# Performance work log

Measured on AMD Instinct MI355X. Metric: run time of the kernel, lower is better.

Reference implementation:

```python
import jax, jax.numpy as jnp
import numpy as np

D_MODEL = 2048
N_HEADS = 16
KV_HEADS = 4
HEAD_DIM = D_MODEL // N_HEADS            # 128
GROUP = N_HEADS // KV_HEADS              # 4
KV_WIDTH = KV_HEADS * HEAD_DIM           # 512
B, T = 2, 2048


def setup_inputs() -> dict:
    key = jax.random.key(0)
    ks = jax.random.split(key, 5)
    s = 0.02
    x = jax.random.normal(ks[0], (B, T, D_MODEL), dtype=jnp.float32)
    attn_mask = jnp.tril(jnp.ones((T, T), dtype=bool))  # causal
    qkv_w = jax.random.normal(ks[1], (D_MODEL, D_MODEL + 2 * KV_WIDTH), dtype=jnp.float32) * s
    qkv_b = jax.random.normal(ks[2], (D_MODEL + 2 * KV_WIDTH,), dtype=jnp.float32) * s
    proj_w = jax.random.normal(ks[3], (D_MODEL, D_MODEL), dtype=jnp.float32) * s
    proj_b = jax.random.normal(ks[4], (D_MODEL,), dtype=jnp.float32) * s
    return {"x": x, "attn_mask": attn_mask, "qkv_w": qkv_w, "qkv_b": qkv_b,
            "proj_w": proj_w, "proj_b": proj_b}


def reference(x, attn_mask, qkv_w, qkv_b, proj_w, proj_b):
    b, t, c = x.shape
    qkv = x @ qkv_w + qkv_b                               # [b,t,3072]
    q = qkv[..., :D_MODEL]
    k = qkv[..., D_MODEL:D_MODEL + KV_WIDTH]
    v = qkv[..., D_MODEL + KV_WIDTH:]
    # q: [b, kv_heads, group, t, d]; k,v: [b, kv_heads, t, d]
    q = q.reshape(b, t, KV_HEADS, GROUP, HEAD_DIM).transpose(0, 2, 3, 1, 4)
    k = k.reshape(b, t, KV_HEADS, HEAD_DIM).transpose(0, 2, 1, 3)
    v = v.reshape(b, t, KV_HEADS, HEAD_DIM).transpose(0, 2, 1, 3)
    scale = 1.0 / jnp.sqrt(jnp.asarray(HEAD_DIM, dtype=x.dtype))
    att = jnp.einsum('bkgtd,bksd->bkgts', q, k) * scale   # [b,kv,g,t,t]
    att = jnp.where(attn_mask, att, jnp.asarray(-jnp.inf, dtype=att.dtype))
    att = jax.nn.softmax(att, axis=-1)
    out = jnp.einsum('bkgts,bksd->bkgtd', att, v)         # [b,kv,g,t,d]
    out = out.transpose(0, 3, 1, 2, 4).reshape(b, t, c)
    return out @ proj_w + proj_b
```

## Files before the change

### kernel.cpp

```cpp
#include <hip/hip_runtime.h>
#include <cstdint>
#include <cstddef>

#define D_MODEL 2048
#define T_SEQ   2048
#define BATCH   2
#define N_HEADS 16
#define KV_HEADS 4
#define HEAD_DIM 128
#define QKV_N   3072
#define ROWS    (BATCH * T_SEQ)

typedef float  floatx4 __attribute__((ext_vector_type(4)));
typedef short  shortx8 __attribute__((ext_vector_type(8)));
typedef __bf16 bf16x8  __attribute__((ext_vector_type(8)));

typedef const void __attribute__((address_space(1))) gvoid_t;
typedef void __attribute__((address_space(3)))       svoid_t;

__device__ __forceinline__ floatx4 mfma16(shortx8 a, shortx8 b, floatx4 c) {
  return __builtin_amdgcn_mfma_f32_16x16x32_bf16(
      __builtin_bit_cast(bf16x8, a), __builtin_bit_cast(bf16x8, b), c, 0, 0, 0);
}

__device__ __forceinline__ unsigned short f2bf(float f) {
  union { float f; unsigned int u; } v; v.f = f;
  unsigned int u = v.u;
  u += 0x7fffu + ((u >> 16) & 1u);
  return (unsigned short)(u >> 16);
}

__device__ __forceinline__ unsigned short f2bf_hw(float f) {
  return __builtin_bit_cast(unsigned short, (__bf16)f);
}

__global__ void cvt_x(const float* __restrict__ in, unsigned short* __restrict__ out, int n4) {
  int i = blockIdx.x * blockDim.x + threadIdx.x;
  if (i >= n4) return;
  float4 v = ((const float4*)in)[i];
  ushort4 o;
  o.x = f2bf(v.x); o.y = f2bf(v.y); o.z = f2bf(v.z); o.w = f2bf(v.w);
  ((ushort4*)out)[i] = o;
}

__global__ void transpose_cvt(const float* __restrict__ W, unsigned short* __restrict__ Wt,
                              int K, int N) {
  __shared__ float tile[32][33];
  int n0 = blockIdx.x * 32, k0 = blockIdx.y * 32;
  int tx = threadIdx.x, ty = threadIdx.y;
  #pragma unroll
  for (int i = 0; i < 32; i += 8)
    tile[ty + i][tx] = W[(size_t)(k0 + ty + i) * N + n0 + tx];
  __syncthreads();
  #pragma unroll
  for (int i = 0; i < 32; i += 8)
    Wt[(size_t)(n0 + ty + i) * K + k0 + tx] = f2bf(tile[tx][ty + i]);
}

__global__ void build_kt(const unsigned short* __restrict__ qkv, unsigned short* __restrict__ kst) {
  int o = blockIdx.x * blockDim.x + threadIdx.x;
  int t   = o & 2047;
  int d8  = (o >> 11) & 15;
  int kvh = (o >> 15) & 3;
  int b   = o >> 17;
  uint4 v = *(const uint4*)(qkv + (size_t)(b * T_SEQ + t) * QKV_N
                            + D_MODEL + kvh * HEAD_DIM + d8 * 8);
  *(uint4*)(kst + (size_t)o * 8) = v;
}

__global__ void build_vt(const unsigned short* __restrict__ qkv, unsigned short* __restrict__ vst) {
  int o = blockIdx.x * blockDim.x + threadIdx.x;
  int d   = o & 127;
  int t8  = (o >> 7) & 255;
  int kvh = (o >> 15) & 3;
  int b   = o >> 17;
  const unsigned short* src = qkv + (size_t)(b * T_SEQ + t8 * 8) * QKV_N
                              + D_MODEL + 512 + kvh * HEAD_DIM + d;
  union { unsigned short s[8]; uint4 v; } tmp;
  #pragma unroll
  for (int j = 0; j < 8; ++j) tmp.s[j] = src[(size_t)j * QKV_N];
  *(uint4*)(vst + (size_t)o * 8) = tmp.v;
}

__global__ __launch_bounds__(512, 2) void gemm256(
    const unsigned short* __restrict__ A,
    const unsigned short* __restrict__ Bt,
    const float* __restrict__ bias,
    void* __restrict__ Cout,
    int M, int N, int K, int c_bf16)
{
  __shared__ __align__(16) unsigned short lds[65536];
  const int tid  = threadIdx.x;
  const int wave = tid >> 6, lane = tid & 63;
  const int quad = lane >> 4, l16 = lane & 15;
  const int wr = wave >> 2, wc = wave & 3;
  const int bm = blockIdx.y * 256, bn = blockIdx.x * 256;
  const int NT = K >> 6;

  const int r0 = tid >> 3;
  const int cx = (tid & 7) ^ (r0 & 7);
  const size_t K64 = (size_t)64 * K;
  const unsigned short* a_src = A  + (size_t)(bm + r0) * K + cx * 8;
  const unsigned short* b_src = Bt + (size_t)(bn + r0) * K + cx * 8;
  const int wOff = wave * 512;

  #define LDSA_(buf, half) (lds + (((buf) << 1) + (half)) * 8192)
  #define LDSB_(buf, half) (lds + 32768 + (((buf) << 1) + (half)) * 8192)
  #define KOFF(h, t) ((size_t)(h) * 128 * K + (size_t)(t) * 64)
  #define STAGE(srcbase, ldshalf, koff) do {                                          \
    __builtin_amdgcn_global_load_lds((gvoid_t*)((srcbase) + (koff)),                  \
        (svoid_t*)((ldshalf) + wOff), 16, 0, 0);                                      \
    __builtin_amdgcn_global_load_lds((gvoid_t*)((srcbase) + (koff) + K64),            \
        (svoid_t*)((ldshalf) + wOff + 4096), 16, 0, 0);                               \
  } while (0)

  const int rowA = (wr * 64 + l16) * 64;
  const int rowB = (wc * 32 + l16) * 64;
  const int xo0 = ((quad)     ^ (l16 & 7)) * 8;
  const int xo1 = ((4 + quad) ^ (l16 & 7)) * 8;

  floatx4 acc[8][4] = {};
  shortx8 Afr[4][2];
  shortx8 Bfr[4][2];

  STAGE(a_src, LDSA_(0, 0), KOFF(0, 0));
  STAGE(b_src, LDSB_(0, 0), KOFF(0, 0));
  STAGE(b_src, LDSB_(0, 1), KOFF(1, 0));
  STAGE(a_src, LDSA_(0, 1), KOFF(1, 0));
  if (NT > 1) {
    STAGE(a_src, LDSA_(1, 0), KOFF(0, 1));
    STAGE(b_src, LDSB_(1, 0), KOFF(0, 1));
    STAGE(b_src, LDSB_(1, 1), KOFF(1, 1));
  }

  for (int t = 0; t < NT; ++t) {
    const int buf = t & 1;
    unsigned short* sA0 = LDSA_(buf, 0);
    unsigned short* sA1 = LDSA_(buf, 1);
    unsigned short* sB0 = LDSB_(buf, 0);
    unsigned short* sB1 = LDSB_(buf, 1);

    if (t == NT - 1) asm volatile("s_waitcnt vmcnt(0)" ::: "memory");
    else             asm volatile("s_waitcnt vmcnt(6)" ::: "memory");
    __builtin_amdgcn_s_barrier();
    #pragma unroll
    for (int mi = 0; mi < 4; ++mi) {
      Afr[mi][0] = *(const shortx8*)(sA0 + rowA + mi * 1024 + xo0);
      Afr[mi][1] = *(const shortx8*)(sA0 + rowA + mi * 1024 + xo1);
    }
    #pragma unroll
    for (int ni = 0; ni < 2; ++ni) {
      Bfr[ni][0] = *(const shortx8*)(sB0 + rowB + ni * 1024 + xo0);
      Bfr[ni][1] = *(const shortx8*)(sB0 + rowB + ni * 1024 + xo1);
    }
    if (t + 1 < NT) STAGE(a_src, LDSA_(buf ^ 1, 1), KOFF(1, t + 1));
    asm volatile("s_waitcnt lgkmcnt(0)" ::: "memory");
    __builtin_amdgcn_s_setprio(1);
    #pragma unroll
    for (int ks = 0; ks < 2; ++ks)
      #pragma unroll
      for (int mi = 0; mi < 4; ++mi)
        #pragma unroll
        for (int ni = 0; ni < 2; ++ni)
          acc[mi][ni] = mfma16(Afr[mi][ks], Bfr[ni][ks], acc[mi][ni]);
    __builtin_amdgcn_s_setprio(0);
    __builtin_amdgcn_s_barrier();

    #pragma unroll
    for (int ni = 0; ni < 2; ++ni) {
      Bfr[2 + ni][0] = *(const shortx8*)(sB1 + rowB + ni * 1024 + xo0);
      Bfr[2 + ni][1] = *(const shortx8*)(sB1 + rowB + ni * 1024 + xo1);
    }
    if (t + 2 < NT) STAGE(a_src, LDSA_(buf, 0), KOFF(0, t + 2));
    __builtin_amdgcn_s_barrier();
    asm volatile("s_waitcnt lgkmcnt(0)" ::: "memory");
    __builtin_amdgcn_s_setprio(1);
    #pragma unroll
    for (int ks = 0; ks < 2; ++ks)
      #pragma unroll
      for (int mi = 0; mi < 4; ++mi)
        #pragma unroll
        for (int ni = 0; ni < 2; ++ni)
          acc[mi][2 + ni] = mfma16(Afr[mi][ks], Bfr[2 + ni][ks], acc[mi][2 + ni]);
    __builtin_amdgcn_s_setprio(0);
    __builtin_amdgcn_s_barrier();

    #pragma unroll
    for (int mi = 0; mi < 4; ++mi) {
      Afr[mi][0] = *(const shortx8*)(sA1 + rowA + mi * 1024 + xo0);
      Afr[mi][1] = *(const shortx8*)(sA1 + rowA + mi * 1024 + xo1);
    }
    if (t + 2 < NT) STAGE(b_src, LDSB_(buf, 0), KOFF(0, t + 2));
    __builtin_amdgcn_s_barrier();
    asm volatile("s_waitcnt lgkmcnt(0)" ::: "memory");
    __builtin_amdgcn_s_setprio(1);
    #pragma unroll
    for (int ks = 0; ks < 2; ++ks)
      #pragma unroll
      for (int mi = 0; mi < 4; ++mi)
        #pragma unroll
        for (int ni = 0; ni < 2; ++ni)
          acc[4 + mi][2 + ni] = mfma16(Afr[mi][ks], Bfr[2 + ni][ks], acc[4 + mi][2 + ni]);
    __builtin_amdgcn_s_setprio(0);
    __builtin_amdgcn_s_barrier();

    if (t + 2 < NT) STAGE(b_src, LDSB_(buf, 1), KOFF(1, t + 2));
    __builtin_amdgcn_s_barrier();
    __builtin_amdgcn_s_setprio(1);
    #pragma unroll
    for (int ks = 0; ks < 2; ++ks)
      #pragma unroll
      for (int mi = 0; mi < 4; ++mi)
        #pragma unroll
        for (int ni = 0; ni < 2; ++ni)
          acc[4 + mi][ni] = mfma16(Afr[mi][ks], Bfr[ni][ks], acc[4 + mi][ni]);
    __builtin_amdgcn_s_setprio(0);
    __builtin_amdgcn_s_barrier();
  }

  #pragma unroll
  for (int mi = 0; mi < 8; ++mi) {
    const int row = bm + (mi >> 2) * 128 + wr * 64 + (mi & 3) * 16 + quad * 4;
    #pragma unroll
    for (int ni = 0; ni < 4; ++ni) {
      const int col = bn + (ni >> 1) * 128 + wc * 32 + (ni & 1) * 16 + l16;
      const float bv = bias[col];
      #pragma unroll
      for (int r = 0; r < 4; ++r) {
        float v = acc[mi][ni][r] + bv;
        if (c_bf16)
          ((unsigned short*)Cout)[(size_t)(row + r) * N + col] = f2bf_hw(v);
        else
          ((float*)Cout)[(size_t)(row + r) * N + col] = v;
      }
    }
  }
  #undef LDSA_
  #undef LDSB_
  #undef KOFF
  #undef STAGE
}

__global__ __launch_bounds__(512, 4) void attn_kernel(
    const unsigned short* __restrict__ qkv,
    const unsigned short* __restrict__ kst,
    const unsigned short* __restrict__ vst,
    unsigned short* __restrict__ aout)
{
  __shared__ __align__(16) unsigned short sK[2][16 * 64 * 8];
  __shared__ __align__(16) unsigned short sV[2][8 * 128 * 8];
  __shared__ __align__(16) unsigned short sP[8][4 * 16 * 8];

  const int tid  = threadIdx.x;
  const int wave = tid >> 6, lane = tid & 63;
  const int split = wave >> 2, g = wave & 3;
  const int quad = lane >> 4, l16 = lane & 15;
  const int head = blockIdx.y, b = blockIdx.z;
  const int kvh = head >> 2;
  const float cf = 0.08838834764831845f * 1.4426950408889634f;
  const float THR = 25.0f;

  const unsigned short* kbase = kst + (size_t)((b * KV_HEADS + kvh) * 16) * 2048 * 8;
  const unsigned short* vbase = vst + (size_t)((b * KV_HEADS + kvh) * 256) * 128 * 8;
  unsigned short* sPw = sP[wave];

  float* mrgO  = (float*)&sK[0][0];
  float* mrgML = (float*)&sV[0][0];

  #define STAGE_KV(sp, kb_) do {                                               \
    _Pragma("unroll")                                                          \
    for (int it_ = 0; it_ < 4; ++it_) {                                        \
      const int c_ = it_ * 4 + g;                                              \
      __builtin_amdgcn_global_load_lds(                                        \
          (gvoid_t*)(kbase + ((size_t)c_ * 2048 + (kb_)) * 8 + lane * 8),      \
          (svoid_t*)(&sK[sp][c_ * 512]), 16, 0, 0);                            \
    }                                                                          \
    const unsigned short* vt_ = vbase + (size_t)((kb_) >> 3) * 128 * 8;        \
    _Pragma("unroll")                                                          \
    for (int it_ = 0; it_ < 4; ++it_) {                                        \
      const int c_ = it_ * 4 + g;                                              \
      __builtin_amdgcn_global_load_lds(                                        \
          (gvoid_t*)(vt_ + c_ * 512 + lane * 8),                               \
          (svoid_t*)(&sV[sp][c_ * 512]), 16, 0, 0);                            \
    }                                                                          \
  } while (0)

  #pragma unroll 1
  for (int half = 0; half < 2; ++half) {
    const int qt = half ? blockIdx.x : (31 - blockIdx.x);
    const int q0 = qt * 64;

    shortx8 qf[4];
    {
      const unsigned short* qp = qkv + (size_t)(b * T_SEQ + q0 + g * 16 + l16) * QKV_N
                                 + head * HEAD_DIM + quad * 8;
      #pragma unroll
      for (int ks = 0; ks < 4; ++ks)
        qf[ks] = *(const shortx8*)(qp + ks * 32);
    }

    float m_i[4], l_i[4];
    #pragma unroll
    for (int r = 0; r < 4; ++r) { m_i[r] = -__builtin_inff(); l_i[r] = 0.f; }
    floatx4 o_acc[8] = {};

    const int J = (qt >> 1) + 1;
    for (int j = 0; j < J; ++j) {
      const int kt = 2 * j + split;
      const bool act = (kt <= qt);

      __builtin_amdgcn_s_barrier();
      if (act) STAGE_KV(split, kt * 64);
      asm volatile("s_waitcnt vmcnt(0)" ::: "memory");
      __builtin_amdgcn_s_barrier();

      if (act) {
        floatx4 s[4] = {};
        __builtin_amdgcn_s_setprio(1);
        #pragma unroll
        for (int ks = 0; ks < 4; ++ks) {
          #pragma unroll
          for (int ct = 0; ct < 4; ++ct) {
            shortx8 kf = *(const shortx8*)&sK[split][((ks * 4 + quad) * 64 + ct * 16 + l16) * 8];
            s[ct] = mfma16(qf[ks], kf, s[ct]);
          }
        }
        __builtin_amdgcn_s_setprio(0);

        if (kt == qt) {
          const int qrow = q0 + g * 16 + quad * 4;
          const int kb = kt * 64;
          #pragma unroll
          for (int ct = 0; ct < 4; ++ct) {
            const int kcol = kb + ct * 16 + l16;
            #pragma unroll
            for (int r = 0; r < 4; ++r)
              if (kcol > qrow + r) s[ct][r] = -__builtin_inff();
          }
        }

        float mx[4];
        #pragma unroll
        for (int r = 0; r < 4; ++r) {
          float m = fmaxf(fmaxf(s[0][r], s[1][r]), fmaxf(s[2][r], s[3][r]));
          m = fmaxf(m, __shfl_xor(m, 1));
          m = fmaxf(m, __shfl_xor(m, 2));
          m = fmaxf(m, __shfl_xor(m, 4));
          m = fmaxf(m, __shfl_xor(m, 8));
          mx[r] = m;
        }

        if (__ballot((mx[0] > m_i[0] + THR) || (mx[1] > m_i[1] + THR) ||
                     (mx[2] > m_i[2] + THR) || (mx[3] > m_i[3] + THR))) {
          float alpha_r[4];
          #pragma unroll
          for (int r = 0; r < 4; ++r) {
            const float newm = fmaxf(m_i[r], mx[r]);
            alpha_r[r] = exp2f((m_i[r] - newm) * cf);
            m_i[r] = newm;
            l_i[r] *= alpha_r[r];
          }
          #pragma unroll
          for (int nt = 0; nt < 8; ++nt)
            #pragma unroll
            for (int r = 0; r < 4; ++r) o_acc[nt][r] *= alpha_r[r];
        }

        #pragma unroll
        for (int r = 0; r < 4; ++r) {
          const float nmc = m_i[r] * cf;
          float p0 = exp2f(fmaf(s[0][r], cf, -nmc));
          float p1 = exp2f(fmaf(s[1][r], cf, -nmc));
          float p2 = exp2f(fmaf(s[2][r], cf, -nmc));
          float p3 = exp2f(fmaf(s[3][r], cf, -nmc));
          s[0][r] = p0; s[1][r] = p1; s[2][r] = p2; s[3][r] = p3;
          l_i[r] += (p0 + p1) + (p2 + p3);
        }

        #pragma unroll
        for (int c = 0; c < 2; ++c) {
          #pragma unroll
          for (int ctl = 0; ctl < 2; ++ctl) {
            const int ct = c * 2 + ctl;
            #pragma unroll
            for (int r = 0; r < 4; ++r)
              sPw[((ctl * 2 + (l16 >> 3)) * 16 + quad * 4 + r) * 8 + (l16 & 7)] =
                  f2bf_hw(s[ct][r]);
          }
          __asm__ __volatile__("s_waitcnt lgkmcnt(0)" ::: "memory");
          shortx8 pf = *(const shortx8*)&sPw[(quad * 16 + l16) * 8];
          __builtin_amdgcn_s_setprio(1);
          #pragma unroll
          for (int nt = 0; nt < 8; ++nt) {
            shortx8 vf = *(const shortx8*)&sV[split][((c * 4 + quad) * 128 + nt * 16 + l16) * 8];
            o_acc[nt] = mfma16(pf, vf, o_acc[nt]);
          }
          __builtin_amdgcn_s_setprio(0);
        }
      }
    }

    __builtin_amdgcn_s_barrier();
    if (split == 1) {
      #pragma unroll
      for (int nt = 0; nt < 8; ++nt)
        #pragma unroll
        for (int r = 0; r < 4; ++r)
          mrgO[g * 2048 + (quad * 4 + r) * 128 + nt * 16 + l16] = o_acc[nt][r];
      #pragma unroll
      for (int r = 0; r < 4; ++r) {
        mrgML[(g * 64 + lane) * 8 + r * 2]     = m_i[r];
        mrgML[(g * 64 + lane) * 8 + r * 2 + 1] = l_i[r];
      }
    }
    asm volatile("s_waitcnt lgkmcnt(0)" ::: "memory");
    __builtin_amdgcn_s_barrier();

    if (split == 0) {
      float lm[4], a0[4], a1[4];
      #pragma unroll
      for (int r = 0; r < 4; ++r) {
        const float m1 = mrgML[(g * 64 + lane) * 8 + r * 2];
        const float l1 = mrgML[(g * 64 + lane) * 8 + r * 2 + 1];
        const float M = fmaxf(m_i[r], m1);
        a0[r] = exp2f((m_i[r] - M) * cf);
        a1[r] = exp2f((m1 - M) * cf);
        lm[r] = a0[r] * l_i[r] + a1[r] * l1;
      }
      #pragma unroll
      for (int nt = 0; nt < 8; ++nt)
        #pragma unroll
        for (int r = 0; r < 4; ++r)
          o_acc[nt][r] = a0[r] * o_acc[nt][r]
                       + a1[r] * mrgO[g * 2048 + (quad * 4 + r) * 128 + nt * 16 + l16];

      const int trow = q0 + g * 16 + quad * 4;
      #pragma unroll
      for (int r = 0; r < 4; ++r) {
        float l = lm[r];
        l += __shfl_xor(l, 1);
        l += __shfl_xor(l, 2);
        l += __shfl_xor(l, 4);
        l += __shfl_xor(l, 8);
        const float inv = 1.f / l;
        #pragma unroll
        for (int nt = 0; nt < 8; ++nt) {
          aout[(size_t)(b * T_SEQ + trow + r) * D_MODEL + head * HEAD_DIM + nt * 16 + l16] =
              f2bf_hw(o_acc[nt][r] * inv);
        }
      }
    }
  }
  #undef STAGE_KV
}

extern "C" void kernel_launch(void* const* d_in, const int* in_sizes, int n_in,
                              void* d_out, int out_size, void* d_ws, size_t ws_size,
                              hipStream_t stream) {
  const float* x      = (const float*)d_in[0];
  const float* qkv_w  = (const float*)d_in[2];
  const float* qkv_b  = (const float*)d_in[3];
  const float* proj_w = (const float*)d_in[4];
  const float* proj_b = (const float*)d_in[5];
  float* out = (float*)d_out;

  char* ws = (char*)d_ws;
  unsigned short* x_bf    = (unsigned short*)(ws);
  unsigned short* qkvw_t  = (unsigned short*)(ws + (size_t)16777216);
  unsigned short* projw_t = (unsigned short*)(ws + (size_t)29360128);
  unsigned short* qkvbuf  = (unsigned short*)(ws + (size_t)37748736);
  unsigned short* vstaged = (unsigned short*)(ws + (size_t)62914560);
  unsigned short* kstaged = qkvw_t;
  unsigned short* attn_out = x_bf;

  cvt_x<<<(ROWS * D_MODEL / 4 + 255) / 256, 256, 0, stream>>>(x, x_bf, ROWS * D_MODEL / 4);
  transpose_cvt<<<dim3(QKV_N / 32, D_MODEL / 32), dim3(32, 8), 0, stream>>>(qkv_w, qkvw_t, D_MODEL, QKV_N);
  transpose_cvt<<<dim3(D_MODEL / 32, D_MODEL / 32), dim3(32, 8), 0, stream>>>(proj_w, projw_t, D_MODEL, D_MODEL);
  gemm256<<<dim3(QKV_N / 256, ROWS / 256), 512, 0, stream>>>(
      x_bf, qkvw_t, qkv_b, (void*)qkvbuf, ROWS, QKV_N, D_MODEL, 1);
  build_kt<<<1024, 256, 0, stream>>>(qkvbuf, kstaged);
  build_vt<<<1024, 256, 0, stream>>>(qkvbuf, vstaged);
  attn_kernel<<<dim3(16, N_HEADS, BATCH), 512, 0, stream>>>(qkvbuf, kstaged, vstaged, attn_out);
  gemm256<<<dim3(D_MODEL / 256, ROWS / 256), 512, 0, stream>>>(
      attn_out, projw_t, proj_b, (void*)out, ROWS, D_MODEL, D_MODEL, 0);
}
```

Baseline: 329.6 us.

## Prefetch next K/V tile into registers and skip row-max shuffles unless rescaling

Replaces the direct global-to-LDS K/V staging with a register prefetch. The next tile's K/V is loaded into registers while the current tile is written to LDS and computed, so global load latency overlaps with the MFMA and softmax work instead of stalling at a vmcnt(0) wait each iteration. The lazy-rescale check now uses each lane's local max, and the cross-lane shuffle reduction runs only when a rescale is triggered. This adds VGPR pressure (8 uint4 per thread) that may lower occupancy. The per-lane threshold check is still correct because any lane exceeding the threshold triggers the ballot.

```diff
diff --git a/kernel.cpp b/kernel.cpp
--- a/kernel.cpp
+++ b/kernel.cpp
@@ -267,21 +267,19 @@
   float* mrgO  = (float*)&sK[0][0];
   float* mrgML = (float*)&sV[0][0];
 
-  #define STAGE_KV(sp, kb_) do {                                               \
+  uint4 rgK[4], rgV[4];
+
+  #define LOADREGS(kb_) do {                                                   \
     _Pragma("unroll")                                                          \
     for (int it_ = 0; it_ < 4; ++it_) {                                        \
       const int c_ = it_ * 4 + g;                                              \
-      __builtin_amdgcn_global_load_lds(                                        \
-          (gvoid_t*)(kbase + ((size_t)c_ * 2048 + (kb_)) * 8 + lane * 8),      \
-          (svoid_t*)(&sK[sp][c_ * 512]), 16, 0, 0);                            \
+      rgK[it_] = *(const uint4*)(kbase + ((size_t)c_ * 2048 + (kb_)) * 8 + lane * 8); \
     }                                                                          \
     const unsigned short* vt_ = vbase + (size_t)((kb_) >> 3) * 128 * 8;        \
     _Pragma("unroll")                                                          \
     for (int it_ = 0; it_ < 4; ++it_) {                                        \
       const int c_ = it_ * 4 + g;                                              \
-      __builtin_amdgcn_global_load_lds(                                        \
-          (gvoid_t*)(vt_ + c_ * 512 + lane * 8),                               \
-          (svoid_t*)(&sV[sp][c_ * 512]), 16, 0, 0);                            \
+      rgV[it_] = *(const uint4*)(vt_ + c_ * 512 + lane * 8);                   \
     }                                                                          \
   } while (0)
 
@@ -304,14 +302,24 @@
     for (int r = 0; r < 4; ++r) { m_i[r] = -__builtin_inff(); l_i[r] = 0.f; }
     floatx4 o_acc[8] = {};
 
+    if (split <= qt) LOADREGS(split * 64);
+
     const int J = (qt >> 1) + 1;
     for (int j = 0; j < J; ++j) {
       const int kt = 2 * j + split;
       const bool act = (kt <= qt);
 
       __builtin_amdgcn_s_barrier();
-      if (act) STAGE_KV(split, kt * 64);
-      asm volatile("s_waitcnt vmcnt(0)" ::: "memory");
+      if (act) {
+        #pragma unroll
+        for (int it = 0; it < 4; ++it) {
+          const int c = it * 4 + g;
+          *(uint4*)&sK[split][c * 512 + lane * 8] = rgK[it];
+          *(uint4*)&sV[split][c * 512 + lane * 8] = rgV[it];
+        }
+      }
+      { const int ktn = kt + 2; if (ktn <= qt) LOADREGS(ktn * 64); }
+      asm volatile("s_waitcnt lgkmcnt(0)" ::: "memory");
       __builtin_amdgcn_s_barrier();
 
       if (act) {
@@ -339,23 +347,23 @@
           }
         }
 
-        float mx[4];
+        float lmx[4];
+        bool over = false;
         #pragma unroll
         for (int r = 0; r < 4; ++r) {
-          float m = fmaxf(fmaxf(s[0][r], s[1][r]), fmaxf(s[2][r], s[3][r]));
-          m = fmaxf(m, __shfl_xor(m, 1));
-          m = fmaxf(m, __shfl_xor(m, 2));
-          m = fmaxf(m, __shfl_xor(m, 4));
-          m = fmaxf(m, __shfl_xor(m, 8));
-          mx[r] = m;
-        }
-
-        if (__ballot((mx[0] > m_i[0] + THR) || (mx[1] > m_i[1] + THR) ||
-                     (mx[2] > m_i[2] + THR) || (mx[3] > m_i[3] + THR))) {
+          lmx[r] = fmaxf(fmaxf(s[0][r], s[1][r]), fmaxf(s[2][r], s[3][r]));
+          over = over || (lmx[r] > m_i[r] + THR);
+        }
+        if (__ballot(over)) {
           float alpha_r[4];
           #pragma unroll
           for (int r = 0; r < 4; ++r) {
-            const float newm = fmaxf(m_i[r], mx[r]);
+            float m = lmx[r];
+            m = fmaxf(m, __shfl_xor(m, 1));
+            m = fmaxf(m, __shfl_xor(m, 2));
+            m = fmaxf(m, __shfl_xor(m, 4));
+            m = fmaxf(m, __shfl_xor(m, 8));
+            const float newm = fmaxf(m_i[r], m);
             alpha_r[r] = exp2f((m_i[r] - newm) * cf);
             m_i[r] = newm;
             l_i[r] *= alpha_r[r];
@@ -451,7 +459,7 @@
       }
     }
   }
-  #undef STAGE_KV
+  #undef LOADREGS
 }
 
 extern "C" void kernel_launch(void* const* d_in, const int* in_sizes, int n_in,
```

Result: slower. 458.0 us (+38.9%).

## Template GEMM N-tile width, use 256x128 tiles for projection, overlap V load in attention

Applied to the files above, without the earlier changes.

The GEMM kernel is templated on the B-tile width, so the output projection runs with 256x128 tiles. That doubles its block count (128 blocks to 256) for better CU occupancy on the small N=2048 problem. In the attention kernel, the wait on the K/V load is relaxed to vmcnt(4) so QK^T and softmax can start while V is still arriving, with a full wait and barrier added before the PV stage. The row-max shuffle reduction now runs only when the ballot shows a rescale is needed, which risks a subtle correctness issue if the per-lane threshold check is weaker than the full-row check.

```diff
diff --git a/kernel.cpp b/kernel.cpp
--- a/kernel.cpp
+++ b/kernel.cpp
@@ -82,6 +82,7 @@
   *(uint4*)(vst + (size_t)o * 8) = tmp.v;
 }
 
+template<int NB>
 __global__ __launch_bounds__(512, 2) void gemm256(
     const unsigned short* __restrict__ A,
     const unsigned short* __restrict__ Bt,
@@ -89,12 +90,12 @@
     void* __restrict__ Cout,
     int M, int N, int K, int c_bf16)
 {
-  __shared__ __align__(16) unsigned short lds[65536];
+  __shared__ __align__(16) unsigned short lds[32768 + NB * 16384];
   const int tid  = threadIdx.x;
   const int wave = tid >> 6, lane = tid & 63;
   const int quad = lane >> 4, l16 = lane & 15;
   const int wr = wave >> 2, wc = wave & 3;
-  const int bm = blockIdx.y * 256, bn = blockIdx.x * 256;
+  const int bm = blockIdx.y * 256, bn = blockIdx.x * (NB * 128);
   const int NT = K >> 6;
 
   const int r0 = tid >> 3;
@@ -105,32 +106,40 @@
   const int wOff = wave * 512;
 
   #define LDSA_(buf, half) (lds + (((buf) << 1) + (half)) * 8192)
-  #define LDSB_(buf, half) (lds + 32768 + (((buf) << 1) + (half)) * 8192)
-  #define KOFF(h, t) ((size_t)(h) * 128 * K + (size_t)(t) * 64)
-  #define STAGE(srcbase, ldshalf, koff) do {                                          \
+  #define LDSB_(buf, half) (lds + 32768 + (((buf) << 1) + (half)) * (NB * 4096))
+  #define KOFFA(h, t) ((size_t)(h) * 128 * K + (size_t)(t) * 64)
+  #define KOFFB(h, t) ((size_t)(h) * (64 * NB) * K + (size_t)(t) * 64)
+  #define STAGE_A(srcbase, ldshalf, koff) do {                                        \
     __builtin_amdgcn_global_load_lds((gvoid_t*)((srcbase) + (koff)),                  \
         (svoid_t*)((ldshalf) + wOff), 16, 0, 0);                                      \
     __builtin_amdgcn_global_load_lds((gvoid_t*)((srcbase) + (koff) + K64),            \
         (svoid_t*)((ldshalf) + wOff + 4096), 16, 0, 0);                               \
   } while (0)
+  #define STAGE_B(srcbase, ldshalf, koff) do {                                        \
+    _Pragma("unroll")                                                                 \
+    for (int j_ = 0; j_ < NB; ++j_)                                                   \
+      __builtin_amdgcn_global_load_lds(                                               \
+          (gvoid_t*)((srcbase) + (koff) + (size_t)j_ * K64),                          \
+          (svoid_t*)((ldshalf) + wOff + j_ * 4096), 16, 0, 0);                        \
+  } while (0)
 
   const int rowA = (wr * 64 + l16) * 64;
-  const int rowB = (wc * 32 + l16) * 64;
+  const int rowB = (wc * (16 * NB) + l16) * 64;
   const int xo0 = ((quad)     ^ (l16 & 7)) * 8;
   const int xo1 = ((4 + quad) ^ (l16 & 7)) * 8;
 
-  floatx4 acc[8][4] = {};
+  floatx4 acc[8][2 * NB] = {};
   shortx8 Afr[4][2];
-  shortx8 Bfr[4][2];
-
-  STAGE(a_src, LDSA_(0, 0), KOFF(0, 0));
-  STAGE(b_src, LDSB_(0, 0), KOFF(0, 0));
-  STAGE(b_src, LDSB_(0, 1), KOFF(1, 0));
-  STAGE(a_src, LDSA_(0, 1), KOFF(1, 0));
+  shortx8 Bfr[2 * NB][2];
+
+  STAGE_A(a_src, LDSA_(0, 0), KOFFA(0, 0));
+  STAGE_B(b_src, LDSB_(0, 0), KOFFB(0, 0));
+  STAGE_B(b_src, LDSB_(0, 1), KOFFB(1, 0));
+  STAGE_A(a_src, LDSA_(0, 1), KOFFA(1, 0));
   if (NT > 1) {
-    STAGE(a_src, LDSA_(1, 0), KOFF(0, 1));
-    STAGE(b_src, LDSB_(1, 0), KOFF(0, 1));
-    STAGE(b_src, LDSB_(1, 1), KOFF(1, 1));
+    STAGE_A(a_src, LDSA_(1, 0), KOFFA(0, 1));
+    STAGE_B(b_src, LDSB_(1, 0), KOFFB(0, 1));
+    STAGE_B(b_src, LDSB_(1, 1), KOFFB(1, 1));
   }
 
   for (int t = 0; t < NT; ++t) {
@@ -141,7 +150,8 @@
     unsigned short* sB1 = LDSB_(buf, 1);
 
     if (t == NT - 1) asm volatile("s_waitcnt vmcnt(0)" ::: "memory");
-    else             asm volatile("s_waitcnt vmcnt(6)" ::: "memory");
+    else if constexpr (NB == 2) asm volatile("s_waitcnt vmcnt(6)" ::: "memory");
+    else                        asm volatile("s_waitcnt vmcnt(4)" ::: "memory");
     __builtin_amdgcn_s_barrier();
     #pragma unroll
     for (int mi = 0; mi < 4; ++mi) {
@@ -149,11 +159,11 @@
       Afr[mi][1] = *(const shortx8*)(sA0 + rowA + mi * 1024 + xo1);
     }
     #pragma unroll
-    for (int ni = 0; ni < 2; ++ni) {
+    for (int ni = 0; ni < NB; ++ni) {
       Bfr[ni][0] = *(const shortx8*)(sB0 + rowB + ni * 1024 + xo0);
       Bfr[ni][1] = *(const shortx8*)(sB0 + rowB + ni * 1024 + xo1);
     }
-    if (t + 1 < NT) STAGE(a_src, LDSA_(buf ^ 1, 1), KOFF(1, t + 1));
+    if (t + 1 < NT) STAGE_A(a_src, LDSA_(buf ^ 1, 1), KOFFA(1, t + 1));
     asm volatile("s_waitcnt lgkmcnt(0)" ::: "memory");
     __builtin_amdgcn_s_setprio(1);
     #pragma unroll
@@ -161,17 +171,17 @@
       #pragma unroll
       for (int mi = 0; mi < 4; ++mi)
         #pragma unroll
-        for (int ni = 0; ni < 2; ++ni)
+        for (int ni = 0; ni < NB; ++ni)
           acc[mi][ni] = mfma16(Afr[mi][ks], Bfr[ni][ks], acc[mi][ni]);
     __builtin_amdgcn_s_setprio(0);
     __builtin_amdgcn_s_barrier();
 
     #pragma unroll
-    for (int ni = 0; ni < 2; ++ni) {
-      Bfr[2 + ni][0] = *(const shortx8*)(sB1 + rowB + ni * 1024 + xo0);
-      Bfr[2 + ni][1] = *(const shortx8*)(sB1 + rowB + ni * 1024 + xo1);
-    }
-    if (t + 2 < NT) STAGE(a_src, LDSA_(buf, 0), KOFF(0, t + 2));
+    for (int ni = 0; ni < NB; ++ni) {
+      Bfr[NB + ni][0] = *(const shortx8*)(sB1 + rowB + ni * 1024 + xo0);
+      Bfr[NB + ni][1] = *(const shortx8*)(sB1 + rowB + ni * 1024 + xo1);
+    }
+    if (t + 2 < NT) STAGE_A(a_src, LDSA_(buf, 0), KOFFA(0, t + 2));
     __builtin_amdgcn_s_barrier();
     asm volatile("s_waitcnt lgkmcnt(0)" ::: "memory");
     __builtin_amdgcn_s_setprio(1);
@@ -180,8 +190,8 @@
       #pragma unroll
       for (int mi = 0; mi < 4; ++mi)
         #pragma unroll
-        for (int ni = 0; ni < 2; ++ni)
-          acc[mi][2 + ni] = mfma16(Afr[mi][ks], Bfr[2 + ni][ks], acc[mi][2 + ni]);
+        for (int ni = 0; ni < NB; ++ni)
+          acc[mi][NB + ni] = mfma16(Afr[mi][ks], Bfr[NB + ni][ks], acc[mi][NB + ni]);
     __builtin_amdgcn_s_setprio(0);
     __builtin_amdgcn_s_barrier();
 
@@ -190,7 +200,7 @@
       Afr[mi][0] = *(const shortx8*)(sA1 + rowA + mi * 1024 + xo0);
       Afr[mi][1] = *(const shortx8*)(sA1 + rowA + mi * 1024 + xo1);
     }
-    if (t + 2 < NT) STAGE(b_src, LDSB_(buf, 0), KOFF(0, t + 2));
+    if (t + 2 < NT) STAGE_B(b_src, LDSB_(buf, 0), KOFFB(0, t + 2));
     __builtin_amdgcn_s_barrier();
     asm volatile("s_waitcnt lgkmcnt(0)" ::: "memory");
     __builtin_amdgcn_s_setprio(1);
@@ -199,12 +209,12 @@
       #pragma unroll
       for (int mi = 0; mi < 4; ++mi)
         #pragma unroll
-        for (int ni = 0; ni < 2; ++ni)
-          acc[4 + mi][2 + ni] = mfma16(Afr[mi][ks], Bfr[2 + ni][ks], acc[4 + mi][2 + ni]);
+        for (int ni = 0; ni < NB; ++ni)
+          acc[4 + mi][NB + ni] = mfma16(Afr[mi][ks], Bfr[NB + ni][ks], acc[4 + mi][NB + ni]);
     __builtin_amdgcn_s_setprio(0);
     __builtin_amdgcn_s_barrier();
 
-    if (t + 2 < NT) STAGE(b_src, LDSB_(buf, 1), KOFF(1, t + 2));
+    if (t + 2 < NT) STAGE_B(b_src, LDSB_(buf, 1), KOFFB(1, t + 2));
     __builtin_amdgcn_s_barrier();
     __builtin_amdgcn_s_setprio(1);
     #pragma unroll
@@ -212,7 +222,7 @@
       #pragma unroll
       for (int mi = 0; mi < 4; ++mi)
         #pragma unroll
-        for (int ni = 0; ni < 2; ++ni)
+        for (int ni = 0; ni < NB; ++ni)
           acc[4 + mi][ni] = mfma16(Afr[mi][ks], Bfr[ni][ks], acc[4 + mi][ni]);
     __builtin_amdgcn_s_setprio(0);
     __builtin_amdgcn_s_barrier();
@@ -222,8 +232,8 @@
   for (int mi = 0; mi < 8; ++mi) {
     const int row = bm + (mi >> 2) * 128 + wr * 64 + (mi & 3) * 16 + quad * 4;
     #pragma unroll
-    for (int ni = 0; ni < 4; ++ni) {
-      const int col = bn + (ni >> 1) * 128 + wc * 32 + (ni & 1) * 16 + l16;
+    for (int ni = 0; ni < 2 * NB; ++ni) {
+      const int col = bn + (ni / NB) * (64 * NB) + wc * (16 * NB) + (ni % NB) * 16 + l16;
       const float bv = bias[col];
       #pragma unroll
       for (int r = 0; r < 4; ++r) {
@@ -237,8 +247,10 @@
   }
   #undef LDSA_
   #undef LDSB_
-  #undef KOFF
-  #undef STAGE
+  #undef KOFFA
+  #undef KOFFB
+  #undef STAGE_A
+  #undef STAGE_B
 }
 
 __global__ __launch_bounds__(512, 4) void attn_kernel(
@@ -308,14 +320,14 @@
     for (int j = 0; j < J; ++j) {
       const int kt = 2 * j + split;
       const bool act = (kt <= qt);
+      floatx4 s[4] = {};
 
       __builtin_amdgcn_s_barrier();
       if (act) STAGE_KV(split, kt * 64);
-      asm volatile("s_waitcnt vmcnt(0)" ::: "memory");
+      asm volatile("s_waitcnt vmcnt(4)" ::: "memory");
       __builtin_amdgcn_s_barrier();
 
       if (act) {
-        floatx4 s[4] = {};
         __builtin_amdgcn_s_setprio(1);
         #pragma unroll
         for (int ks = 0; ks < 4; ++ks) {
@@ -339,23 +351,23 @@
           }
         }
 
-        float mx[4];
+        float lmx[4];
+        bool over = false;
         #pragma unroll
         for (int r = 0; r < 4; ++r) {
-          float m = fmaxf(fmaxf(s[0][r], s[1][r]), fmaxf(s[2][r], s[3][r]));
-          m = fmaxf(m, __shfl_xor(m, 1));
-          m = fmaxf(m, __shfl_xor(m, 2));
-          m = fmaxf(m, __shfl_xor(m, 4));
-          m = fmaxf(m, __shfl_xor(m, 8));
-          mx[r] = m;
-        }
-
-        if (__ballot((mx[0] > m_i[0] + THR) || (mx[1] > m_i[1] + THR) ||
-                     (mx[2] > m_i[2] + THR) || (mx[3] > m_i[3] + THR))) {
+          lmx[r] = fmaxf(fmaxf(s[0][r], s[1][r]), fmaxf(s[2][r], s[3][r]));
+          over = over || (lmx[r] > m_i[r] + THR);
+        }
+        if (__ballot(over)) {
           float alpha_r[4];
           #pragma unroll
           for (int r = 0; r < 4; ++r) {
-            const float newm = fmaxf(m_i[r], mx[r]);
+            float m = lmx[r];
+            m = fmaxf(m, __shfl_xor(m, 1));
+            m = fmaxf(m, __shfl_xor(m, 2));
+            m = fmaxf(m, __shfl_xor(m, 4));
+            m = fmaxf(m, __shfl_xor(m, 8));
+            const float newm = fmaxf(m_i[r], m);
             alpha_r[r] = exp2f((m_i[r] - newm) * cf);
             m_i[r] = newm;
             l_i[r] *= alpha_r[r];
@@ -376,7 +388,12 @@
           s[0][r] = p0; s[1][r] = p1; s[2][r] = p2; s[3][r] = p3;
           l_i[r] += (p0 + p1) + (p2 + p3);
         }
-
+      }
+
+      asm volatile("s_waitcnt vmcnt(0)" ::: "memory");
+      __builtin_amdgcn_s_barrier();
+
+      if (act) {
         #pragma unroll
         for (int c = 0; c < 2; ++c) {
           #pragma unroll
@@ -476,11 +493,11 @@
   cvt_x<<<(ROWS * D_MODEL / 4 + 255) / 256, 256, 0, stream>>>(x, x_bf, ROWS * D_MODEL / 4);
   transpose_cvt<<<dim3(QKV_N / 32, D_MODEL / 32), dim3(32, 8), 0, stream>>>(qkv_w, qkvw_t, D_MODEL, QKV_N);
   transpose_cvt<<<dim3(D_MODEL / 32, D_MODEL / 32), dim3(32, 8), 0, stream>>>(proj_w, projw_t, D_MODEL, D_MODEL);
-  gemm256<<<dim3(QKV_N / 256, ROWS / 256), 512, 0, stream>>>(
+  gemm256<2><<<dim3(QKV_N / 256, ROWS / 256), 512, 0, stream>>>(
       x_bf, qkvw_t, qkv_b, (void*)qkvbuf, ROWS, QKV_N, D_MODEL, 1);
   build_kt<<<1024, 256, 0, stream>>>(qkvbuf, kstaged);
   build_vt<<<1024, 256, 0, stream>>>(qkvbuf, vstaged);
   attn_kernel<<<dim3(16, N_HEADS, BATCH), 512, 0, stream>>>(qkvbuf, kstaged, vstaged, attn_out);
-  gemm256<<<dim3(D_MODEL / 256, ROWS / 256), 512, 0, stream>>>(
+  gemm256<1><<<dim3(D_MODEL / 128, ROWS / 256), 512, 0, stream>>>(
       attn_out, projw_t, proj_b, (void*)out, ROWS, D_MODEL, D_MODEL, 0);
 }
```

Measured after the change: 311.5 us. 5.5% less time.
